# Performance work log

Measured on AMD Instinct MI355X. Metric: run time of the kernel, lower is better.

Reference implementation:

```python
import jax, jax.numpy as jnp
import numpy as np

AB = 8            # activation quant bits
NOISE_LEVEL = 0.1
CY_SCALE = 2.0    # stands in for args.cy_scale
B, IN, H = 8192, 512, 512


def _fake_quant(x, bits, sign):
    # forward: clip/clamp then round-to-grid; backward (STE) handled elsewhere
    if sign:
        delta = 1.0 / (2.0 ** (bits - 1))
        xc = jnp.clip(x, -1.0 + delta, 1.0 - delta)
        scale = 2.0 ** (bits - 1)
    else:
        xc = jnp.clip(x, 0.0, 1.0)
        scale = 2.0 ** bits
    q = jnp.round(xc * scale) / scale
    # STE: identity gradient w.r.t. x
    return x + jax.lax.stop_gradient(q - x)


def setup_inputs() -> dict:
    key = jax.random.key(0)
    ks = jax.random.split(key, 11)
    return {
        "input": jax.random.normal(ks[0], (B, IN), jnp.float32),
        "hx": jax.random.normal(ks[1], (B, H), jnp.float32),
        "cx": jax.random.normal(ks[2], (B, H), jnp.float32),
        "weight_ih": jax.random.normal(ks[3], (4 * H, IN), jnp.float32),
        "weight_hh": jax.random.normal(ks[4], (4 * H, H), jnp.float32),
        "bias_ih": jax.random.normal(ks[5], (4 * H,), jnp.float32),
        "bias_hh": jax.random.normal(ks[6], (4 * H,), jnp.float32),
        "noise_ih": jax.random.normal(ks[7], (IN, 4 * H), jnp.float32),
        "noise_hh": jax.random.normal(ks[8], (H, 4 * H), jnp.float32),
        "noise_bias_ih": jax.random.normal(ks[9], (4 * H,), jnp.float32),
        "noise_bias_hh": jax.random.normal(ks[10], (4 * H,), jnp.float32),
    }


def reference(input, hx, cx, weight_ih, weight_hh, bias_ih, bias_hh,
              noise_ih, noise_hh, noise_bias_ih, noise_bias_hh):
    # noisy weights: noise = randn * w.max() * noise_level (raw randn passed in)
    w_ih = weight_ih.T + noise_ih * (jnp.max(weight_ih) * NOISE_LEVEL)   # [IN,4H]
    w_hh = weight_hh.T + noise_hh * (jnp.max(weight_hh) * NOISE_LEVEL)   # [H,4H]
    b_ih = bias_ih + noise_bias_ih * (jnp.max(bias_ih) * NOISE_LEVEL)
    b_hh = bias_hh + noise_bias_hh * (jnp.max(bias_hh) * NOISE_LEVEL)

    gates = input @ w_ih + b_ih + hx @ w_hh + b_hh                        # [B,4H]
    ingate, forgetgate, cellgate, outgate = jnp.split(gates, 4, axis=1)

    ingate = _fake_quant(jax.nn.sigmoid(ingate), AB, False)
    forgetgate = _fake_quant(jax.nn.sigmoid(forgetgate), AB, False)
    cellgate = _fake_quant(jnp.tanh(cellgate), AB, True)
    outgate = _fake_quant(jax.nn.sigmoid(outgate), AB, False)

    cy = _fake_quant(
        (_fake_quant(forgetgate * cx, AB, True)
         + _fake_quant(ingate * cellgate, AB, True)) / CY_SCALE,
        AB, True)
    hy = _fake_quant(
        outgate * _fake_quant(jnp.tanh(cy * CY_SCALE), AB, True),
        AB, True)
    return (hy, cy)
```

## Files before the change

### kernel.cpp

```cpp
#include <hip/hip_runtime.h>
#include <cstdint>

typedef unsigned short u16;
typedef __bf16 bf16x8 __attribute__((ext_vector_type(8)));
typedef float f32x4 __attribute__((ext_vector_type(4)));

#define NB 8192
#define HD 512
#define KD 1024
#define ND 2048
#define HY_OFF (NB * HD)
#define NT 32

__device__ __forceinline__ u16 f2bf(float f) {
  unsigned u = __float_as_uint(f);
  u += 0x7FFFu + ((u >> 16) & 1u);
  return (u16)(u >> 16);
}
__device__ __forceinline__ float bf2f(u16 h) {
  return __uint_as_float(((unsigned)h) << 16);
}
__device__ __forceinline__ void atomicMaxF(float* a, float v) {
  if (v >= 0.f) atomicMax((int*)a, __float_as_int(v));
  else          atomicMin((unsigned int*)a, __float_as_uint(v));
}
__device__ __forceinline__ float fq_u(float x) {
  float xc = fminf(fmaxf(x, 0.0f), 1.0f);
  return rintf(xc * 256.0f) * (1.0f / 256.0f);
}
__device__ __forceinline__ float fq_s(float x) {
  const float lim = 1.0f - 1.0f / 128.0f;
  float xc = fminf(fmaxf(x, -lim), lim);
  return rintf(xc * 128.0f) * (1.0f / 128.0f);
}
__device__ __forceinline__ float sigm(float x) { return 1.0f / (1.0f + expf(-x)); }

__device__ __forceinline__ void gload_lds16(const u16* g, u16* l) {
  __builtin_amdgcn_global_load_lds(
      (const __attribute__((address_space(1))) void*)g,
      (__attribute__((address_space(3))) void*)l, 16, 0, 0);
}

__global__ __launch_bounds__(256) void k_prep_max(
    const float* __restrict__ w_ih, const float* __restrict__ w_hh,
    const float* __restrict__ b_ih, const float* __restrict__ b_hh,
    float* __restrict__ maxes) {
  int bid = blockIdx.x;
  const float* src; int slot, base;
  if (bid < 1024)      { src = w_ih; slot = 0; base = bid * 1024; }
  else if (bid < 2048) { src = w_hh; slot = 1; base = (bid - 1024) * 1024; }
  else if (bid < 2050) { src = b_ih; slot = 2; base = (bid - 2048) * 1024; }
  else                 { src = b_hh; slot = 3; base = (bid - 2050) * 1024; }
  float m = -INFINITY;
  for (int i = threadIdx.x; i < 1024; i += 256) m = fmaxf(m, src[base + i]);
  for (int k = 1; k < 64; k <<= 1) m = fmaxf(m, __shfl_xor(m, k, 64));
  __shared__ float sm[4];
  if ((threadIdx.x & 63) == 0) sm[threadIdx.x >> 6] = m;
  __syncthreads();
  if (threadIdx.x == 0) {
    m = fmaxf(fmaxf(sm[0], sm[1]), fmaxf(sm[2], sm[3]));
    atomicMaxF(&maxes[slot], m);
  }
}

__global__ __launch_bounds__(256) void k_prep_build(
    const float* __restrict__ input, const float* __restrict__ hx,
    const float* __restrict__ w_ih, const float* __restrict__ w_hh,
    const float* __restrict__ n_ih, const float* __restrict__ n_hh,
    const float* __restrict__ b_ih, const float* __restrict__ b_hh,
    const float* __restrict__ nb_ih, const float* __restrict__ nb_hh,
    const float* __restrict__ maxes,
    u16* __restrict__ Xhi, u16* __restrict__ Xlo,
    u16* __restrict__ Whi, u16* __restrict__ Wlo,
    float* __restrict__ biasC) {
  const int bid = blockIdx.x;
  if (bid < 2048) {
    const int total4 = NB * KD / 4;
    for (int e4 = bid * 256 + threadIdx.x; e4 < total4; e4 += 2048 * 256) {
      int row = e4 >> 8;
      int c4  = e4 & 255;
      float4 v = (c4 < 128)
          ? reinterpret_cast<const float4*>(input)[row * 128 + c4]
          : reinterpret_cast<const float4*>(hx)[row * 128 + (c4 - 128)];
      float xs[4] = {v.x, v.y, v.z, v.w};
      ushort4 hi, lo;
      u16 h0 = f2bf(xs[0]); u16 l0 = f2bf(xs[0] - bf2f(h0));
      u16 h1 = f2bf(xs[1]); u16 l1 = f2bf(xs[1] - bf2f(h1));
      u16 h2 = f2bf(xs[2]); u16 l2 = f2bf(xs[2] - bf2f(h2));
      u16 h3 = f2bf(xs[3]); u16 l3 = f2bf(xs[3] - bf2f(h3));
      hi.x = h0; hi.y = h1; hi.z = h2; hi.w = h3;
      lo.x = l0; lo.y = l1; lo.z = l2; lo.w = l3;
      reinterpret_cast<ushort4*>(Xhi)[e4] = hi;
      reinterpret_cast<ushort4*>(Xlo)[e4] = lo;
    }
  } else if (bid < 2560) {
    __shared__ float nT[256][17];
    const int w  = bid - 2048;
    const int cg = w >> 2, kb = w & 3;
    const int j0 = cg * 16;
    const int g  = ((j0 >> 7) & 1) * 2 + ((j0 >> 4) & 1);
    const int hb = ((j0 >> 8) << 2) | ((j0 >> 5) & 3);
    const int col0 = g * 512 + (hb << 4);
    const int k0 = kb * 256;
    {
      const int cl = threadIdx.x & 15;
      const int kr = threadIdx.x >> 4;
#pragma unroll 4
      for (int i = 0; i < 16; ++i) {
        const int k = k0 + kr + 16 * i;
        nT[kr + 16 * i][cl] = (k < 512) ? n_ih[k * ND + col0 + cl]
                                        : n_hh[(k - 512) * ND + col0 + cl];
      }
    }
    __syncthreads();
    const float s_ih = maxes[0] * 0.1f, s_hh = maxes[1] * 0.1f;
    const int c  = threadIdx.x >> 4;
    const int kl = threadIdx.x & 15;
    const int colL = col0 + c;
    const int j = j0 + c;
#pragma unroll
    for (int kk = 0; kk < 4; ++kk) {
      const int k = k0 + kk * 64 + kl * 4;
      float4 wv; float s;
      if (k < 512) {
        wv = reinterpret_cast<const float4*>(w_ih)[(colL * 512 + k) >> 2];
        s = s_ih;
      } else {
        wv = reinterpret_cast<const float4*>(w_hh)[(colL * 512 + k - 512) >> 2];
        s = s_hh;
      }
      const int kt = k - k0;
      float xs[4] = {wv.x + nT[kt + 0][c] * s, wv.y + nT[kt + 1][c] * s,
                     wv.z + nT[kt + 2][c] * s, wv.w + nT[kt + 3][c] * s};
      ushort4 hi, lo;
      u16 h0 = f2bf(xs[0]); u16 l0 = f2bf(xs[0] - bf2f(h0));
      u16 h1 = f2bf(xs[1]); u16 l1 = f2bf(xs[1] - bf2f(h1));
      u16 h2 = f2bf(xs[2]); u16 l2 = f2bf(xs[2] - bf2f(h2));
      u16 h3 = f2bf(xs[3]); u16 l3 = f2bf(xs[3] - bf2f(h3));
      hi.x = h0; hi.y = h1; hi.z = h2; hi.w = h3;
      lo.x = l0; lo.y = l1; lo.z = l2; lo.w = l3;
      reinterpret_cast<ushort4*>(Whi)[(j * KD + k) >> 2] = hi;
      reinterpret_cast<ushort4*>(Wlo)[(j * KD + k) >> 2] = lo;
    }
  } else {
    int j = (bid - 2560) * 256 + threadIdx.x;
    if (j < ND) {
      int g  = ((j >> 7) & 1) * 2 + ((j >> 4) & 1);
      int hb = ((j >> 8) << 2) | ((j >> 5) & 3);
      int col = g * 512 + (hb << 4) + (j & 15);
      biasC[j] = b_ih[col] + nb_ih[col] * (maxes[2] * 0.1f)
               + b_hh[col] + nb_hh[col] * (maxes[3] * 0.1f);
    }
  }
}

__global__ __launch_bounds__(512, 2) void k_gemm_lstm(
    const u16* __restrict__ Xhi, const u16* __restrict__ Xlo,
    const u16* __restrict__ Whi, const u16* __restrict__ Wlo,
    const float* __restrict__ biasC, const float* __restrict__ cx,
    float* __restrict__ out) {
  __shared__ u16 L[2][4][8192];
  const int tid  = threadIdx.x;
  const int lane = tid & 63, wid = tid >> 6;
  const int wr = wid >> 2, wc = wid & 3;
  const int lr = lane & 15, lg = lane >> 4;
  const int xcd = blockIdx.x & 7, tt = blockIdx.x >> 3;
  const int bm = ((xcd >> 1) << 3) | (tt & 7);
  const int bn = ((xcd & 1) << 2) | (tt >> 3);
  const int mbase = bm * 256, nbase = bn * 256;

  const int l8 = lane >> 3, l7 = lane & 7;
  const int csrc  = l7 ^ l8;
  const int srow  = wid * 16 + 2 * l8 + (csrc >> 2);
  const int skoff = (csrc & 3) * 8;
  const int sdst  = wid * 512;

  const int fro = (lr >> 1) * 64 + ((((lr & 1) << 2) | lg) ^ ((lr >> 1) & 7)) * 8;

  f32x4 acc[8][4] = {};
  bf16x8 afr[4][2];
  bf16x8 bfr[2][2][2];

#define STAGE(V, SLOT, BUF, HALF)                                             \
  {                                                                           \
    const u16* arr_ = (BUF) == 0 ? Xhi : (BUF) == 1 ? Xlo                     \
                      : (BUF) == 2 ? Whi : Wlo;                               \
    const int gb_ = ((BUF) < 2 ? mbase : nbase) + (HALF) * 128 + srow;        \
    gload_lds16(arr_ + (size_t)gb_ * KD + (V) * 32 + skoff,                   \
                &L[(SLOT)][(BUF)][(HALF) * 4096 + sdst]);                     \
  }

#define STAGE8(V, SLOT)                                                       \
  {                                                                           \
    STAGE(V, SLOT, 0, 0); STAGE(V, SLOT, 1, 0);                               \
    STAGE(V, SLOT, 2, 0); STAGE(V, SLOT, 3, 0);                               \
    STAGE(V, SLOT, 2, 1); STAGE(V, SLOT, 3, 1);                               \
    STAGE(V, SLOT, 0, 1); STAGE(V, SLOT, 1, 1);                               \
  }

#define PHX(S, MH, NH, LOADA, LOADB)                                          \
  {                                                                           \
    if (LOADA) {                                                              \
      _Pragma("unroll") for (int m2 = 0; m2 < 4; ++m2) {                      \
        const int ab = ((MH) * 128 + wr * 64 + m2 * 16) * 32 + fro;           \
        afr[m2][0] = *reinterpret_cast<const bf16x8*>(&L[S][0][ab]);          \
        afr[m2][1] = *reinterpret_cast<const bf16x8*>(&L[S][1][ab]);          \
      }                                                                       \
    }                                                                         \
    if (LOADB) {                                                              \
      _Pragma("unroll") for (int n2 = 0; n2 < 2; ++n2) {                      \
        const int bb = ((NH) * 128 + wc * 32 + n2 * 16) * 32 + fro;           \
        bfr[(NH)][n2][0] = *reinterpret_cast<const bf16x8*>(&L[S][2][bb]);    \
        bfr[(NH)][n2][1] = *reinterpret_cast<const bf16x8*>(&L[S][3][bb]);    \
      }                                                                       \
    }                                                                         \
    __builtin_amdgcn_s_setprio(1);                                            \
    _Pragma("unroll") for (int t = 0; t < 3; ++t)                             \
      _Pragma("unroll") for (int m2 = 0; m2 < 4; ++m2)                        \
        _Pragma("unroll") for (int n2 = 0; n2 < 2; ++n2) {                    \
          f32x4* ac = &acc[(MH) * 4 + m2][(NH) * 2 + n2];                     \
          *ac = __builtin_amdgcn_mfma_f32_16x16x32_bf16(afr[m2][t == 1],      \
                    bfr[(NH)][n2][t == 2], *ac, 0, 0, 0);                     \
        }                                                                     \
    __builtin_amdgcn_s_setprio(0);                                            \
  }

#define TILE(U, S)                                                            \
  STAGE8((U) + 1, (S) ^ 1)                                                    \
  PHX(S, 0, 0, 1, 1)                                                          \
  PHX(S, 0, 1, 0, 1)                                                          \
  PHX(S, 1, 1, 1, 0)                                                          \
  PHX(S, 1, 0, 0, 0)                                                          \
  __syncthreads();

  STAGE8(0, 0)
  __syncthreads();

  for (int u = 0; u < NT - 2; u += 2) {
    TILE(u, 0)
    TILE(u + 1, 1)
  }
  TILE(30, 0)
  PHX(1, 0, 0, 1, 1)
  PHX(1, 0, 1, 0, 1)
  PHX(1, 1, 1, 1, 0)
  PHX(1, 1, 0, 0, 0)

#undef TILE
#undef PHX
#undef STAGE8
#undef STAGE

  const int hb = bn * 4 + wc;
  const int h = hb * 16 + lr;
  float bias[4];
#pragma unroll
  for (int g = 0; g < 4; ++g)
    bias[g] = biasC[bn * 256 + ((g >> 1) * 8 + wc * 2 + (g & 1)) * 16 + lr];
#pragma unroll
  for (int mh = 0; mh < 2; ++mh) {
#pragma unroll
    for (int m2 = 0; m2 < 4; ++m2) {
      const int m = mh * 4 + m2;
#pragma unroll
      for (int r = 0; r < 4; ++r) {
        const int row = mbase + mh * 128 + wr * 64 + m2 * 16 + lg * 4 + r;
        const float gi = acc[m][0][r] + bias[0];
        const float gf = acc[m][1][r] + bias[1];
        const float gc = acc[m][2][r] + bias[2];
        const float go = acc[m][3][r] + bias[3];
        const float ig = fq_u(sigm(gi));
        const float fg = fq_u(sigm(gf));
        const float cg = fq_s(tanhf(gc));
        const float og = fq_u(sigm(go));
        const float cxv = cx[(size_t)row * HD + h];
        const float t1 = fq_s(fg * cxv);
        const float t2 = fq_s(ig * cg);
        const float cyv = fq_s((t1 + t2) * 0.5f);
        const float hyv = fq_s(og * fq_s(tanhf(cyv * 2.0f)));
        out[(size_t)row * HD + h] = hyv;
        out[HY_OFF + (size_t)row * HD + h] = cyv;
      }
    }
  }
}

extern "C" void kernel_launch(void* const* d_in, const int* in_sizes, int n_in,
                              void* d_out, int out_size, void* d_ws, size_t ws_size,
                              hipStream_t stream) {
  const float* input = (const float*)d_in[0];
  const float* hx    = (const float*)d_in[1];
  const float* cx    = (const float*)d_in[2];
  const float* w_ih  = (const float*)d_in[3];
  const float* w_hh  = (const float*)d_in[4];
  const float* b_ih  = (const float*)d_in[5];
  const float* b_hh  = (const float*)d_in[6];
  const float* n_ih  = (const float*)d_in[7];
  const float* n_hh  = (const float*)d_in[8];
  const float* nb_ih = (const float*)d_in[9];
  const float* nb_hh = (const float*)d_in[10];
  float* out = (float*)d_out;

  char* ws = (char*)d_ws;
  float* maxes = (float*)ws;
  u16* Xhi = (u16*)(ws + 256);
  u16* Xlo = (u16*)(ws + 256 + 16777216);
  u16* Whi = (u16*)(ws + 256 + 2 * 16777216);
  u16* Wlo = (u16*)(ws + 256 + 2 * 16777216 + 4194304);
  float* biasC = (float*)(ws + 256 + 2 * 16777216 + 2 * 4194304);

  hipMemsetAsync(maxes, 0xFF, 16, stream);
  hipLaunchKernelGGL(k_prep_max, dim3(2052), dim3(256), 0, stream,
                     w_ih, w_hh, b_ih, b_hh, maxes);
  hipLaunchKernelGGL(k_prep_build, dim3(2568), dim3(256), 0, stream,
                     input, hx, w_ih, w_hh, n_ih, n_hh, b_ih, b_hh,
                     nb_ih, nb_hh, maxes, Xhi, Xlo, Whi, Wlo, biasC);
  hipLaunchKernelGGL(k_gemm_lstm, dim3(256), dim3(512), 0, stream,
                     Xhi, Xlo, Whi, Wlo, biasC, cx, out);
}
```

Measured before the change: 149.7 us.

## Shrink GEMM tiles to 128x128, interleave staged loads with MFMA phases, merge prep

The fused GEMM+LSTM kernel moves from 256x256 tiles with 512 threads to 128x128 tiles with 256 threads. This launches 1024 blocks instead of 256 and halves LDS use per block, aiming for better occupancy and load balance across CUs. Next-tile global-to-LDS loads are now spread between the four MFMA phases, with explicit vmcnt waits and raw barriers replacing __syncthreads, to overlap memory with compute. The X hi/lo split is fused with the max reduction in one prep kernel, and the weight/bias column permutation is changed to a simpler gate layout. The cost is less data reuse per tile, so more global and L2 traffic, and the hand-written waitcnt is fragile.

```diff
diff --git a/kernel.cpp b/kernel.cpp
--- a/kernel.cpp
+++ b/kernel.cpp
@@ -41,38 +41,11 @@
       (__attribute__((address_space(3))) void*)l, 16, 0, 0);
 }
 
-__global__ __launch_bounds__(256) void k_prep_max(
+__global__ __launch_bounds__(256) void k_prep1(
+    const float* __restrict__ input, const float* __restrict__ hx,
     const float* __restrict__ w_ih, const float* __restrict__ w_hh,
     const float* __restrict__ b_ih, const float* __restrict__ b_hh,
-    float* __restrict__ maxes) {
-  int bid = blockIdx.x;
-  const float* src; int slot, base;
-  if (bid < 1024)      { src = w_ih; slot = 0; base = bid * 1024; }
-  else if (bid < 2048) { src = w_hh; slot = 1; base = (bid - 1024) * 1024; }
-  else if (bid < 2050) { src = b_ih; slot = 2; base = (bid - 2048) * 1024; }
-  else                 { src = b_hh; slot = 3; base = (bid - 2050) * 1024; }
-  float m = -INFINITY;
-  for (int i = threadIdx.x; i < 1024; i += 256) m = fmaxf(m, src[base + i]);
-  for (int k = 1; k < 64; k <<= 1) m = fmaxf(m, __shfl_xor(m, k, 64));
-  __shared__ float sm[4];
-  if ((threadIdx.x & 63) == 0) sm[threadIdx.x >> 6] = m;
-  __syncthreads();
-  if (threadIdx.x == 0) {
-    m = fmaxf(fmaxf(sm[0], sm[1]), fmaxf(sm[2], sm[3]));
-    atomicMaxF(&maxes[slot], m);
-  }
-}
-
-__global__ __launch_bounds__(256) void k_prep_build(
-    const float* __restrict__ input, const float* __restrict__ hx,
-    const float* __restrict__ w_ih, const float* __restrict__ w_hh,
-    const float* __restrict__ n_ih, const float* __restrict__ n_hh,
-    const float* __restrict__ b_ih, const float* __restrict__ b_hh,
-    const float* __restrict__ nb_ih, const float* __restrict__ nb_hh,
-    const float* __restrict__ maxes,
-    u16* __restrict__ Xhi, u16* __restrict__ Xlo,
-    u16* __restrict__ Whi, u16* __restrict__ Wlo,
-    float* __restrict__ biasC) {
+    u16* __restrict__ Xhi, u16* __restrict__ Xlo, float* __restrict__ maxes) {
   const int bid = blockIdx.x;
   if (bid < 2048) {
     const int total4 = NB * KD / 4;
@@ -93,13 +66,40 @@
       reinterpret_cast<ushort4*>(Xhi)[e4] = hi;
       reinterpret_cast<ushort4*>(Xlo)[e4] = lo;
     }
-  } else if (bid < 2560) {
+  } else {
+    int mb = bid - 2048;
+    const float* src; int slot, base;
+    if (mb < 1024)      { src = w_ih; slot = 0; base = mb * 1024; }
+    else if (mb < 2048) { src = w_hh; slot = 1; base = (mb - 1024) * 1024; }
+    else if (mb < 2050) { src = b_ih; slot = 2; base = (mb - 2048) * 1024; }
+    else                { src = b_hh; slot = 3; base = (mb - 2050) * 1024; }
+    float m = -INFINITY;
+    for (int i = threadIdx.x; i < 1024; i += 256) m = fmaxf(m, src[base + i]);
+    for (int k = 1; k < 64; k <<= 1) m = fmaxf(m, __shfl_xor(m, k, 64));
+    __shared__ float sm[4];
+    if ((threadIdx.x & 63) == 0) sm[threadIdx.x >> 6] = m;
+    __syncthreads();
+    if (threadIdx.x == 0) {
+      m = fmaxf(fmaxf(sm[0], sm[1]), fmaxf(sm[2], sm[3]));
+      atomicMaxF(&maxes[slot], m);
+    }
+  }
+}
+
+__global__ __launch_bounds__(256) void k_prep2(
+    const float* __restrict__ w_ih, const float* __restrict__ w_hh,
+    const float* __restrict__ n_ih, const float* __restrict__ n_hh,
+    const float* __restrict__ b_ih, const float* __restrict__ b_hh,
+    const float* __restrict__ nb_ih, const float* __restrict__ nb_hh,
+    const float* __restrict__ maxes,
+    u16* __restrict__ Whi, u16* __restrict__ Wlo, float* __restrict__ biasC) {
+  const int bid = blockIdx.x;
+  if (bid < 512) {
     __shared__ float nT[256][17];
-    const int w  = bid - 2048;
-    const int cg = w >> 2, kb = w & 3;
+    const int cg = bid >> 2, kb = bid & 3;
     const int j0 = cg * 16;
-    const int g  = ((j0 >> 7) & 1) * 2 + ((j0 >> 4) & 1);
-    const int hb = ((j0 >> 8) << 2) | ((j0 >> 5) & 3);
+    const int g  = cg & 3;
+    const int hb = cg >> 2;
     const int col0 = g * 512 + (hb << 4);
     const int k0 = kb * 256;
     {
@@ -143,33 +143,32 @@
       reinterpret_cast<ushort4*>(Wlo)[(j * KD + k) >> 2] = lo;
     }
   } else {
-    int j = (bid - 2560) * 256 + threadIdx.x;
+    int j = (bid - 512) * 256 + threadIdx.x;
     if (j < ND) {
-      int g  = ((j >> 7) & 1) * 2 + ((j >> 4) & 1);
-      int hb = ((j >> 8) << 2) | ((j >> 5) & 3);
-      int col = g * 512 + (hb << 4) + (j & 15);
+      int hb = j >> 6, g = (j >> 4) & 3, hl = j & 15;
+      int col = g * 512 + (hb << 4) + hl;
       biasC[j] = b_ih[col] + nb_ih[col] * (maxes[2] * 0.1f)
                + b_hh[col] + nb_hh[col] * (maxes[3] * 0.1f);
     }
   }
 }
 
-__global__ __launch_bounds__(512, 2) void k_gemm_lstm(
+__global__ __launch_bounds__(256, 2) void k_gemm_lstm(
     const u16* __restrict__ Xhi, const u16* __restrict__ Xlo,
     const u16* __restrict__ Whi, const u16* __restrict__ Wlo,
     const float* __restrict__ biasC, const float* __restrict__ cx,
     float* __restrict__ out) {
-  __shared__ u16 L[2][4][8192];
+  __shared__ u16 L[2][4][4096];
   const int tid  = threadIdx.x;
   const int lane = tid & 63, wid = tid >> 6;
-  const int wr = wid >> 2, wc = wid & 3;
+  const int wr = wid >> 1, wc = wid & 1;
   const int lr = lane & 15, lg = lane >> 4;
+  const int l7 = lane & 7, l8 = lane >> 3;
   const int xcd = blockIdx.x & 7, tt = blockIdx.x >> 3;
-  const int bm = ((xcd >> 1) << 3) | (tt & 7);
-  const int bn = ((xcd & 1) << 2) | (tt >> 3);
-  const int mbase = bm * 256, nbase = bn * 256;
-
-  const int l8 = lane >> 3, l7 = lane & 7;
+  const int bm = xcd * 8 + (tt & 7);
+  const int bn = tt >> 3;
+  const int mbase = bm * 128, nbase = bn * 128;
+
   const int csrc  = l7 ^ l8;
   const int srow  = wid * 16 + 2 * l8 + (csrc >> 2);
   const int skoff = (csrc & 3) * 8;
@@ -177,110 +176,94 @@
 
   const int fro = (lr >> 1) * 64 + ((((lr & 1) << 2) | lg) ^ ((lr >> 1) & 7)) * 8;
 
-  f32x4 acc[8][4] = {};
+  f32x4 acc[4][4] = {};
   bf16x8 afr[4][2];
-  bf16x8 bfr[2][2][2];
+  bf16x8 bfrp[2];
 
 #define STAGE(V, SLOT, BUF, HALF)                                             \
   {                                                                           \
     const u16* arr_ = (BUF) == 0 ? Xhi : (BUF) == 1 ? Xlo                     \
                       : (BUF) == 2 ? Whi : Wlo;                               \
-    const int gb_ = ((BUF) < 2 ? mbase : nbase) + (HALF) * 128 + srow;        \
+    const int gb_ = ((BUF) < 2 ? mbase : nbase) + (HALF) * 64 + srow;         \
     gload_lds16(arr_ + (size_t)gb_ * KD + (V) * 32 + skoff,                   \
-                &L[(SLOT)][(BUF)][(HALF) * 4096 + sdst]);                     \
-  }
-
-#define STAGE8(V, SLOT)                                                       \
+                &L[(SLOT)][(BUF)][(HALF) * 2048 + sdst]);                     \
+  }
+
+#define MMPH(S, N2)                                                           \
   {                                                                           \
-    STAGE(V, SLOT, 0, 0); STAGE(V, SLOT, 1, 0);                               \
-    STAGE(V, SLOT, 2, 0); STAGE(V, SLOT, 3, 0);                               \
-    STAGE(V, SLOT, 2, 1); STAGE(V, SLOT, 3, 1);                               \
-    STAGE(V, SLOT, 0, 1); STAGE(V, SLOT, 1, 1);                               \
-  }
-
-#define PHX(S, MH, NH, LOADA, LOADB)                                          \
-  {                                                                           \
-    if (LOADA) {                                                              \
-      _Pragma("unroll") for (int m2 = 0; m2 < 4; ++m2) {                      \
-        const int ab = ((MH) * 128 + wr * 64 + m2 * 16) * 32 + fro;           \
-        afr[m2][0] = *reinterpret_cast<const bf16x8*>(&L[S][0][ab]);          \
-        afr[m2][1] = *reinterpret_cast<const bf16x8*>(&L[S][1][ab]);          \
-      }                                                                       \
-    }                                                                         \
-    if (LOADB) {                                                              \
-      _Pragma("unroll") for (int n2 = 0; n2 < 2; ++n2) {                      \
-        const int bb = ((NH) * 128 + wc * 32 + n2 * 16) * 32 + fro;           \
-        bfr[(NH)][n2][0] = *reinterpret_cast<const bf16x8*>(&L[S][2][bb]);    \
-        bfr[(NH)][n2][1] = *reinterpret_cast<const bf16x8*>(&L[S][3][bb]);    \
-      }                                                                       \
-    }                                                                         \
+    const int bb_ = (wc * 64 + (N2) * 16) * 32 + fro;                         \
+    bfrp[0] = *reinterpret_cast<const bf16x8*>(&L[S][2][bb_]);                \
+    bfrp[1] = *reinterpret_cast<const bf16x8*>(&L[S][3][bb_]);                \
     __builtin_amdgcn_s_setprio(1);                                            \
     _Pragma("unroll") for (int t = 0; t < 3; ++t)                             \
-      _Pragma("unroll") for (int m2 = 0; m2 < 4; ++m2)                        \
-        _Pragma("unroll") for (int n2 = 0; n2 < 2; ++n2) {                    \
-          f32x4* ac = &acc[(MH) * 4 + m2][(NH) * 2 + n2];                     \
-          *ac = __builtin_amdgcn_mfma_f32_16x16x32_bf16(afr[m2][t == 1],      \
-                    bfr[(NH)][n2][t == 2], *ac, 0, 0, 0);                     \
-        }                                                                     \
+      _Pragma("unroll") for (int m2 = 0; m2 < 4; ++m2) {                      \
+        f32x4* ac = &acc[m2][N2];                                             \
+        *ac = __builtin_amdgcn_mfma_f32_16x16x32_bf16(afr[m2][t == 1],        \
+                  bfrp[t == 2], *ac, 0, 0, 0);                                \
+      }                                                                       \
     __builtin_amdgcn_s_setprio(0);                                            \
   }
 
 #define TILE(U, S)                                                            \
-  STAGE8((U) + 1, (S) ^ 1)                                                    \
-  PHX(S, 0, 0, 1, 1)                                                          \
-  PHX(S, 0, 1, 0, 1)                                                          \
-  PHX(S, 1, 1, 1, 0)                                                          \
-  PHX(S, 1, 0, 0, 0)                                                          \
-  __syncthreads();
-
-  STAGE8(0, 0)
-  __syncthreads();
-
-  for (int u = 0; u < NT - 2; u += 2) {
+  {                                                                           \
+    const int Vn = ((U) + 1 > NT - 1) ? (NT - 1) : (U) + 1;                   \
+    STAGE(Vn, (S) ^ 1, 0, 0); STAGE(Vn, (S) ^ 1, 0, 1);                       \
+    asm volatile("s_waitcnt vmcnt(2)" ::: "memory");                          \
+    __builtin_amdgcn_s_barrier();                                             \
+    _Pragma("unroll") for (int m2 = 0; m2 < 4; ++m2) {                        \
+      const int ab_ = (wr * 64 + m2 * 16) * 32 + fro;                         \
+      afr[m2][0] = *reinterpret_cast<const bf16x8*>(&L[S][0][ab_]);           \
+      afr[m2][1] = *reinterpret_cast<const bf16x8*>(&L[S][1][ab_]);           \
+    }                                                                         \
+    MMPH(S, 0)                                                                \
+    STAGE(Vn, (S) ^ 1, 1, 0); STAGE(Vn, (S) ^ 1, 1, 1);                       \
+    MMPH(S, 1)                                                                \
+    STAGE(Vn, (S) ^ 1, 2, 0); STAGE(Vn, (S) ^ 1, 2, 1);                       \
+    MMPH(S, 2)                                                                \
+    STAGE(Vn, (S) ^ 1, 3, 0); STAGE(Vn, (S) ^ 1, 3, 1);                       \
+    MMPH(S, 3)                                                                \
+    __builtin_amdgcn_s_barrier();                                             \
+  }
+
+  STAGE(0, 0, 0, 0); STAGE(0, 0, 0, 1);
+  STAGE(0, 0, 1, 0); STAGE(0, 0, 1, 1);
+  STAGE(0, 0, 2, 0); STAGE(0, 0, 2, 1);
+  STAGE(0, 0, 3, 0); STAGE(0, 0, 3, 1);
+
+  for (int u = 0; u < NT; u += 2) {
     TILE(u, 0)
     TILE(u + 1, 1)
   }
-  TILE(30, 0)
-  PHX(1, 0, 0, 1, 1)
-  PHX(1, 0, 1, 0, 1)
-  PHX(1, 1, 1, 1, 0)
-  PHX(1, 1, 0, 0, 0)
 
 #undef TILE
-#undef PHX
-#undef STAGE8
+#undef MMPH
 #undef STAGE
 
-  const int hb = bn * 4 + wc;
+  const int hb = bn * 2 + wc;
   const int h = hb * 16 + lr;
   float bias[4];
 #pragma unroll
-  for (int g = 0; g < 4; ++g)
-    bias[g] = biasC[bn * 256 + ((g >> 1) * 8 + wc * 2 + (g & 1)) * 16 + lr];
+  for (int g = 0; g < 4; ++g) bias[g] = biasC[hb * 64 + g * 16 + lr];
 #pragma unroll
-  for (int mh = 0; mh < 2; ++mh) {
+  for (int m2 = 0; m2 < 4; ++m2) {
 #pragma unroll
-    for (int m2 = 0; m2 < 4; ++m2) {
-      const int m = mh * 4 + m2;
-#pragma unroll
-      for (int r = 0; r < 4; ++r) {
-        const int row = mbase + mh * 128 + wr * 64 + m2 * 16 + lg * 4 + r;
-        const float gi = acc[m][0][r] + bias[0];
-        const float gf = acc[m][1][r] + bias[1];
-        const float gc = acc[m][2][r] + bias[2];
-        const float go = acc[m][3][r] + bias[3];
-        const float ig = fq_u(sigm(gi));
-        const float fg = fq_u(sigm(gf));
-        const float cg = fq_s(tanhf(gc));
-        const float og = fq_u(sigm(go));
-        const float cxv = cx[(size_t)row * HD + h];
-        const float t1 = fq_s(fg * cxv);
-        const float t2 = fq_s(ig * cg);
-        const float cyv = fq_s((t1 + t2) * 0.5f);
-        const float hyv = fq_s(og * fq_s(tanhf(cyv * 2.0f)));
-        out[(size_t)row * HD + h] = hyv;
-        out[HY_OFF + (size_t)row * HD + h] = cyv;
-      }
+    for (int r = 0; r < 4; ++r) {
+      const int row = mbase + wr * 64 + m2 * 16 + lg * 4 + r;
+      const float gi = acc[m2][0][r] + bias[0];
+      const float gf = acc[m2][1][r] + bias[1];
+      const float gc = acc[m2][2][r] + bias[2];
+      const float go = acc[m2][3][r] + bias[3];
+      const float ig = fq_u(sigm(gi));
+      const float fg = fq_u(sigm(gf));
+      const float cg = fq_s(tanhf(gc));
+      const float og = fq_u(sigm(go));
+      const float cxv = cx[(size_t)row * HD + h];
+      const float t1 = fq_s(fg * cxv);
+      const float t2 = fq_s(ig * cg);
+      const float cyv = fq_s((t1 + t2) * 0.5f);
+      const float hyv = fq_s(og * fq_s(tanhf(cyv * 2.0f)));
+      out[(size_t)row * HD + h] = hyv;
+      out[HY_OFF + (size_t)row * HD + h] = cyv;
     }
   }
 }
@@ -310,11 +293,11 @@
   float* biasC = (float*)(ws + 256 + 2 * 16777216 + 2 * 4194304);
 
   hipMemsetAsync(maxes, 0xFF, 16, stream);
-  hipLaunchKernelGGL(k_prep_max, dim3(2052), dim3(256), 0, stream,
-                     w_ih, w_hh, b_ih, b_hh, maxes);
-  hipLaunchKernelGGL(k_prep_build, dim3(2568), dim3(256), 0, stream,
-                     input, hx, w_ih, w_hh, n_ih, n_hh, b_ih, b_hh,
-                     nb_ih, nb_hh, maxes, Xhi, Xlo, Whi, Wlo, biasC);
-  hipLaunchKernelGGL(k_gemm_lstm, dim3(256), dim3(512), 0, stream,
+  hipLaunchKernelGGL(k_prep1, dim3(4100), dim3(256), 0, stream,
+                     input, hx, w_ih, w_hh, b_ih, b_hh, Xhi, Xlo, maxes);
+  hipLaunchKernelGGL(k_prep2, dim3(520), dim3(256), 0, stream,
+                     w_ih, w_hh, n_ih, n_hh, b_ih, b_hh, nb_ih, nb_hh,
+                     maxes, Whi, Wlo, biasC);
+  hipLaunchKernelGGL(k_gemm_lstm, dim3(1024), dim3(256), 0, stream,
                      Xhi, Xlo, Whi, Wlo, biasC, cx, out);
 }
```

Result: no change. 151.7 us (+1.4%).

## Interleave next-tile staging with MFMA phases and vectorize max reduction

Applied to the files above, without the earlier changes.

The GEMM main loop no longer issues all eight global-to-LDS loads for the next K tile at the start and then syncs once per tile. It spreads the loads across the four compute phases, two at a time, and uses explicit vmcnt waits and s_barrier between phases, so memory traffic overlaps with MFMA work more finely. The max-reduction kernel now reads float4 and launches 514 blocks instead of 2052. The per-phase barriers add synchronization overhead, and correctness depends on the hand-tuned vmcnt counts matching the load order.

```diff
diff --git a/kernel.cpp b/kernel.cpp
--- a/kernel.cpp
+++ b/kernel.cpp
@@ -41,18 +41,21 @@
       (__attribute__((address_space(3))) void*)l, 16, 0, 0);
 }
 
-__global__ __launch_bounds__(256) void k_prep_max(
+__global__ __launch_bounds__(256) void k_max(
     const float* __restrict__ w_ih, const float* __restrict__ w_hh,
     const float* __restrict__ b_ih, const float* __restrict__ b_hh,
     float* __restrict__ maxes) {
-  int bid = blockIdx.x;
-  const float* src; int slot, base;
-  if (bid < 1024)      { src = w_ih; slot = 0; base = bid * 1024; }
-  else if (bid < 2048) { src = w_hh; slot = 1; base = (bid - 1024) * 1024; }
-  else if (bid < 2050) { src = b_ih; slot = 2; base = (bid - 2048) * 1024; }
-  else                 { src = b_hh; slot = 3; base = (bid - 2050) * 1024; }
+  const int bid = blockIdx.x;
+  const float4* src; int slot, base4, n4;
+  if (bid < 256)      { src = (const float4*)w_ih; slot = 0; base4 = bid * 1024; n4 = 1024; }
+  else if (bid < 512) { src = (const float4*)w_hh; slot = 1; base4 = (bid - 256) * 1024; n4 = 1024; }
+  else if (bid == 512){ src = (const float4*)b_ih; slot = 2; base4 = 0; n4 = 512; }
+  else                { src = (const float4*)b_hh; slot = 3; base4 = 0; n4 = 512; }
   float m = -INFINITY;
-  for (int i = threadIdx.x; i < 1024; i += 256) m = fmaxf(m, src[base + i]);
+  for (int i = threadIdx.x; i < n4; i += 256) {
+    float4 v = src[base4 + i];
+    m = fmaxf(m, fmaxf(fmaxf(v.x, v.y), fmaxf(v.z, v.w)));
+  }
   for (int k = 1; k < 64; k <<= 1) m = fmaxf(m, __shfl_xor(m, k, 64));
   __shared__ float sm[4];
   if ((threadIdx.x & 63) == 0) sm[threadIdx.x >> 6] = m;
@@ -63,7 +66,7 @@
   }
 }
 
-__global__ __launch_bounds__(256) void k_prep_build(
+__global__ __launch_bounds__(256) void k_prep(
     const float* __restrict__ input, const float* __restrict__ hx,
     const float* __restrict__ w_ih, const float* __restrict__ w_hh,
     const float* __restrict__ n_ih, const float* __restrict__ n_hh,
@@ -181,39 +184,34 @@
   bf16x8 afr[4][2];
   bf16x8 bfr[2][2][2];
 
-#define STAGE(V, SLOT, BUF, HALF)                                             \
+#define STAGE(V, BUF, HALF)                                                   \
   {                                                                           \
     const u16* arr_ = (BUF) == 0 ? Xhi : (BUF) == 1 ? Xlo                     \
                       : (BUF) == 2 ? Whi : Wlo;                               \
     const int gb_ = ((BUF) < 2 ? mbase : nbase) + (HALF) * 128 + srow;        \
     gload_lds16(arr_ + (size_t)gb_ * KD + (V) * 32 + skoff,                   \
-                &L[(SLOT)][(BUF)][(HALF) * 4096 + sdst]);                     \
-  }
-
-#define STAGE8(V, SLOT)                                                       \
-  {                                                                           \
-    STAGE(V, SLOT, 0, 0); STAGE(V, SLOT, 1, 0);                               \
-    STAGE(V, SLOT, 2, 0); STAGE(V, SLOT, 3, 0);                               \
-    STAGE(V, SLOT, 2, 1); STAGE(V, SLOT, 3, 1);                               \
-    STAGE(V, SLOT, 0, 1); STAGE(V, SLOT, 1, 1);                               \
-  }
-
-#define PHX(S, MH, NH, LOADA, LOADB)                                          \
+                &L[(V) & 1][(BUF)][(HALF) * 4096 + sdst]);                    \
+  }
+
+#define PH(MH, NH, LOADA, LOADB, STAGE_CODE, WAIT_CODE)                       \
   {                                                                           \
     if (LOADA) {                                                              \
       _Pragma("unroll") for (int m2 = 0; m2 < 4; ++m2) {                      \
         const int ab = ((MH) * 128 + wr * 64 + m2 * 16) * 32 + fro;           \
-        afr[m2][0] = *reinterpret_cast<const bf16x8*>(&L[S][0][ab]);          \
-        afr[m2][1] = *reinterpret_cast<const bf16x8*>(&L[S][1][ab]);          \
+        afr[m2][0] = *reinterpret_cast<const bf16x8*>(&L[s][0][ab]);          \
+        afr[m2][1] = *reinterpret_cast<const bf16x8*>(&L[s][1][ab]);          \
       }                                                                       \
     }                                                                         \
     if (LOADB) {                                                              \
       _Pragma("unroll") for (int n2 = 0; n2 < 2; ++n2) {                      \
         const int bb = ((NH) * 128 + wc * 32 + n2 * 16) * 32 + fro;           \
-        bfr[(NH)][n2][0] = *reinterpret_cast<const bf16x8*>(&L[S][2][bb]);    \
-        bfr[(NH)][n2][1] = *reinterpret_cast<const bf16x8*>(&L[S][3][bb]);    \
+        bfr[(NH)][n2][0] = *reinterpret_cast<const bf16x8*>(&L[s][2][bb]);    \
+        bfr[(NH)][n2][1] = *reinterpret_cast<const bf16x8*>(&L[s][3][bb]);    \
       }                                                                       \
     }                                                                         \
+    STAGE_CODE;                                                               \
+    WAIT_CODE;                                                                \
+    __builtin_amdgcn_s_barrier();                                             \
     __builtin_amdgcn_s_setprio(1);                                            \
     _Pragma("unroll") for (int t = 0; t < 3; ++t)                             \
       _Pragma("unroll") for (int m2 = 0; m2 < 4; ++m2)                        \
@@ -223,32 +221,32 @@
                     bfr[(NH)][n2][t == 2], *ac, 0, 0, 0);                     \
         }                                                                     \
     __builtin_amdgcn_s_setprio(0);                                            \
-  }
-
-#define TILE(U, S)                                                            \
-  STAGE8((U) + 1, (S) ^ 1)                                                    \
-  PHX(S, 0, 0, 1, 1)                                                          \
-  PHX(S, 0, 1, 0, 1)                                                          \
-  PHX(S, 1, 1, 1, 0)                                                          \
-  PHX(S, 1, 0, 0, 0)                                                          \
-  __syncthreads();
-
-  STAGE8(0, 0)
-  __syncthreads();
-
-  for (int u = 0; u < NT - 2; u += 2) {
-    TILE(u, 0)
-    TILE(u + 1, 1)
-  }
-  TILE(30, 0)
-  PHX(1, 0, 0, 1, 1)
-  PHX(1, 0, 1, 0, 1)
-  PHX(1, 1, 1, 1, 0)
-  PHX(1, 1, 0, 0, 0)
-
-#undef TILE
-#undef PHX
-#undef STAGE8
+    __builtin_amdgcn_s_barrier();                                             \
+  }
+
+  STAGE(0, 0, 0); STAGE(0, 1, 0);
+  STAGE(0, 2, 0); STAGE(0, 3, 0);
+  STAGE(0, 2, 1); STAGE(0, 3, 1);
+  STAGE(0, 0, 1); STAGE(0, 1, 1);
+  asm volatile("s_waitcnt vmcnt(4)" ::: "memory");
+  __builtin_amdgcn_s_barrier();
+
+  int s = 0;
+  for (int u = 0; u < NT - 1; ++u, s ^= 1) {
+    PH(0, 0, 1, 1, { STAGE(u + 1, 0, 0); STAGE(u + 1, 1, 0); },
+       asm volatile("s_waitcnt vmcnt(4)" ::: "memory"));
+    PH(0, 1, 0, 1, { STAGE(u + 1, 2, 0); STAGE(u + 1, 3, 0); },
+       asm volatile("s_waitcnt vmcnt(4)" ::: "memory"));
+    PH(1, 1, 1, 0, { STAGE(u + 1, 2, 1); STAGE(u + 1, 3, 1); }, );
+    PH(1, 0, 0, 0, { STAGE(u + 1, 0, 1); STAGE(u + 1, 1, 1); },
+       asm volatile("s_waitcnt vmcnt(4)" ::: "memory"));
+  }
+  PH(0, 0, 1, 1, , asm volatile("s_waitcnt vmcnt(2)" ::: "memory"));
+  PH(0, 1, 0, 1, , asm volatile("s_waitcnt vmcnt(0)" ::: "memory"));
+  PH(1, 1, 1, 0, , );
+  PH(1, 0, 0, 0, , );
+
+#undef PH
 #undef STAGE
 
   const int hb = bn * 4 + wc;
@@ -310,9 +308,9 @@
   float* biasC = (float*)(ws + 256 + 2 * 16777216 + 2 * 4194304);
 
   hipMemsetAsync(maxes, 0xFF, 16, stream);
-  hipLaunchKernelGGL(k_prep_max, dim3(2052), dim3(256), 0, stream,
+  hipLaunchKernelGGL(k_max, dim3(514), dim3(256), 0, stream,
                      w_ih, w_hh, b_ih, b_hh, maxes);
-  hipLaunchKernelGGL(k_prep_build, dim3(2568), dim3(256), 0, stream,
+  hipLaunchKernelGGL(k_prep, dim3(2568), dim3(256), 0, stream,
                      input, hx, w_ih, w_hh, n_ih, n_hh, b_ih, b_hh,
                      nb_ih, nb_hh, maxes, Xhi, Xlo, Whi, Wlo, biasC);
   hipLaunchKernelGGL(k_gemm_lstm, dim3(256), dim3(512), 0, stream,
```

Result: faster. 124.1 us (-17.1%).
